# Optimization experiments

Measured on AMD Instinct MI355X. Metric: run time of the kernel, lower is better.

Reference implementation:

```python
import jax, jax.numpy as jnp
import numpy as np

N, A_IN, A_OUT, X_IN, X_OUT, NNODE = 4, 8, 16, 64, 64, 1024


def setup_inputs() -> dict:
    key = jax.random.key(0)
    ks = jax.random.split(key, 32)
    s = 0.02
    inp = {
        'A': jax.random.normal(ks[0], (N, A_IN, NNODE, NNODE), jnp.float32),
        'X': jax.random.normal(ks[1], (N, NNODE, X_IN), jnp.float32),
    }
    # Linear weights stored as (in, out); torch Linear computes x @ W.T with W (out,in)
    for i, k in zip(range(1, 6), ks[2:7]):
        inp[f'A_W{i}'] = jax.random.normal(k, (A_IN, A_OUT), jnp.float32) * s
    inp['A_W6'] = jax.random.normal(ks[7], (X_IN, A_OUT), jnp.float32) * s
    inp['A_W7'] = jax.random.normal(ks[8], (X_IN, A_OUT), jnp.float32) * s
    inp['A_bias'] = jnp.zeros((A_OUT,), jnp.float32)
    for pfx, base in (('X1', 9), ('X2', 16)):
        inp[f'{pfx}_W1'] = jax.random.normal(ks[base], (X_IN, X_OUT), jnp.float32) * s
        inp[f'{pfx}_W2'] = jax.random.normal(ks[base + 1], (X_IN, X_OUT), jnp.float32) * s
        for j in range(3, 7):
            inp[f'{pfx}_W{j}'] = jax.random.normal(ks[base + j - 1], (A_IN, X_OUT), jnp.float32) * s
        inp[f'{pfx}_bias'] = jnp.zeros((X_OUT,), jnp.float32)
    inp['out_W'] = jax.random.normal(ks[23], (A_OUT * X_OUT, X_OUT), jnp.float32) * s
    inp['out_b'] = jnp.zeros((X_OUT,), jnp.float32)
    return inp


def reference(A, X, A_W1, A_W2, A_W3, A_W4, A_W5, A_W6, A_W7, A_bias,
              X1_W1, X1_W2, X1_W3, X1_W4, X1_W5, X1_W6, X1_bias,
              X2_W1, X2_W2, X2_W3, X2_W4, X2_W5, X2_W6, X2_bias,
              out_W, out_b):
    n = A.shape[-1]
    # diag_part: N, n, 1, A_in
    dp = jnp.transpose(jnp.diagonal(A, axis1=-2, axis2=-1), (0, 2, 1))[:, :, None, :]
    mdp = jnp.mean(dp, axis=1, keepdims=True)                 # N,1,1,A_in
    moc = jnp.transpose(jnp.mean(A, axis=-1), (0, 2, 1))[:, :, None, :]  # N,n,1,A_in
    mall = jnp.mean(moc, axis=1, keepdims=True)               # N,1,1,A_in
    mX = jnp.mean(X, axis=-2, keepdims=True)                  # N,1,x_in

    At = jnp.transpose(A, (0, 2, 3, 1)) @ A_W1                # N,n,n,A_out
    At = At + mall @ A_W2
    t3 = moc @ A_W3                                           # N,n,1,A_out (linear commutes with symmetrize)
    At = At + t3 + jnp.swapaxes(t3, 1, 2)
    t6 = X @ A_W6                                             # N,n,A_out
    At = At + t6[:, :, None, :] + t6[:, None, :, :]
    At = At + (mX @ A_W7)[:, None, :, :]
    At = At + A_bias
    At = At + mdp @ A_W4
    t5 = dp @ A_W5
    At = At + t5 + jnp.swapaxes(t5, 1, 2)

    def x_branch(W1, W2, W3, W4, W5, W6, b):
        r = X @ W1 + mX @ W2 + moc[:, :, 0, :] @ W3 + mall[:, 0, :, :] @ W6 + b
        return r + dp[:, :, 0, :] @ W4 + mdp[:, 0, :, :] @ W5  # N,n,x_out

    X1t = x_branch(X1_W1, X1_W2, X1_W3, X1_W4, X1_W5, X1_W6, X1_bias)
    X2t = x_branch(X2_W1, X2_W2, X2_W3, X2_W4, X2_W5, X2_W6, X2_bias)

    out = jnp.einsum('nijs,njt->nist', At, X2t) / n           # N,n,A_out,x_out
    out = out.reshape(out.shape[0], out.shape[1], -1) @ out_W + out_b
    out = out + X1t
    return jnp.transpose(At, (0, 3, 1, 2)), out
```

## Files before the change

### kernel.cpp

```cpp
#include <hip/hip_runtime.h>


#define NB 4
#define CI 8
#define SO 16
#define XD 64
#define NN 1024

typedef unsigned short u16;
typedef unsigned int u32;
typedef float f32x4 __attribute__((ext_vector_type(4)));
typedef short bf16x8 __attribute__((ext_vector_type(8)));

#define WS_MOC    0x000000u
#define WS_DP     0x020000u
#define WS_CONSTA 0x043000u
#define WS_CX1    0x044000u
#define WS_CX2    0x045000u
#define WS_K1     0x048000u
#define WS_C2     0x04C000u
#define WS_PAIRA  0x050000u
#define WS_PAIRAT 0x090000u
#define WS_X1T    0x0D0000u
#define WS_X2TT   0x1D0000u
#define WS_WGT    0x250000u
#define WS_H      0x260000u
#define WS_XPART  0x264000u
#define WS_S2     0x268000u

__device__ __forceinline__ float bf2f(u16 u){ return __uint_as_float(((u32)u) << 16); }
__device__ __forceinline__ u16 f2bf(float f){
    u32 x = __float_as_uint(f);
    x += 0x7fffu + ((x >> 16) & 1u);
    return (u16)(x >> 16);
}

__global__ __launch_bounds__(256) void k_rowstats(const float* __restrict__ A,
                                                  const float* __restrict__ X,
                                                  float* __restrict__ moc,
                                                  float* __restrict__ dpv,
                                                  float* __restrict__ Xpart)
{
    if (blockIdx.x < NB*CI*NN/4) {
        int wave = threadIdx.x >> 6, lane = threadIdx.x & 63;
        int row = blockIdx.x * 4 + wave;
        int i = row & (NN - 1);
        const float* rp = A + (size_t)row * NN;
        f32x4 v0 = *(const f32x4*)(rp + lane * 16);
        f32x4 v1 = *(const f32x4*)(rp + lane * 16 + 4);
        f32x4 v2 = *(const f32x4*)(rp + lane * 16 + 8);
        f32x4 v3 = *(const f32x4*)(rp + lane * 16 + 12);
        float s = 0.f;
        #pragma unroll
        for (int e = 0; e < 4; e++) s += v0[e] + v1[e] + v2[e] + v3[e];
        #pragma unroll
        for (int off = 32; off; off >>= 1) s += __shfl_down(s, off);
        if (lane == 0) {
            moc[row] = s * (1.f / NN);
            dpv[row] = rp[i];
        }
    } else {
        int idx = blockIdx.x - NB*CI*NN/4;
        int b = idx >> 4, seg = idx & 15;
        int g = threadIdx.x >> 6, x = threadIdx.x & 63;
        __shared__ float red[4][64];
        float s = 0.f;
        #pragma unroll
        for (int k = 0; k < 16; k++) {
            int i = seg*64 + g*16 + k;
            s += X[((size_t)b*NN + i)*XD + x];
        }
        red[g][x] = s;
        __syncthreads();
        if (threadIdx.x < 64)
            Xpart[idx*64 + threadIdx.x] =
                red[0][threadIdx.x]+red[1][threadIdx.x]+red[2][threadIdx.x]+red[3][threadIdx.x];
    }
}

__global__ __launch_bounds__(256) void k_batchstats(
    const float* __restrict__ Xpart,
    const float* __restrict__ moc, const float* __restrict__ dpv,
    const float* __restrict__ AW2, const float* __restrict__ AW4, const float* __restrict__ AW7,
    const float* __restrict__ Abias,
    const float* __restrict__ X1W2, const float* __restrict__ X1W5, const float* __restrict__ X1W6,
    const float* __restrict__ X1b,
    const float* __restrict__ X2W2, const float* __restrict__ X2W5, const float* __restrict__ X2W6,
    const float* __restrict__ X2b,
    float* __restrict__ constA_o, float* __restrict__ cx1_o, float* __restrict__ cx2_o)
{
    int b = blockIdx.x, tid = threadIdx.x;
    __shared__ float sdp[8][32], smoc[8][32];
    __shared__ float mdp_s[8], mall_s[8], mx_s[64];
    {
        int c = tid >> 5, rr = tid & 31;
        float pd = 0.f, pm = 0.f;
        for (int i = rr; i < NN; i += 32) {
            pd += dpv[(b*CI + c)*NN + i];
            pm += moc[(b*CI + c)*NN + i];
        }
        sdp[c][rr] = pd; smoc[c][rr] = pm;
    }
    if (tid < 64) {
        float px = 0.f;
        #pragma unroll
        for (int s = 0; s < 16; s++) px += Xpart[(b*16 + s)*64 + tid];
        mx_s[tid] = px * (1.f/NN);
    }
    __syncthreads();
    if (tid < 8) {
        float sd = 0.f, sm = 0.f;
        for (int k = 0; k < 32; k++) { sd += sdp[tid][k]; sm += smoc[tid][k]; }
        mdp_s[tid] = sd * (1.f/NN); mall_s[tid] = sm * (1.f/NN);
    }
    __syncthreads();
    if (tid < SO) {
        float v = Abias[tid];
        #pragma unroll
        for (int c = 0; c < 8; c++)
            v += mall_s[c]*AW2[c*SO+tid] + mdp_s[c]*AW4[c*SO+tid];
        for (int x = 0; x < 64; x++) v += mx_s[x]*AW7[x*SO+tid];
        constA_o[b*SO + tid] = v;
    }
    if (tid < 64) {
        float v1 = X1b[tid], v2 = X2b[tid];
        for (int x = 0; x < 64; x++) {
            float m = mx_s[x];
            v1 += m*X1W2[x*64+tid];
            v2 += m*X2W2[x*64+tid];
        }
        #pragma unroll
        for (int c = 0; c < 8; c++) {
            v1 += mall_s[c]*X1W6[c*64+tid] + mdp_s[c]*X1W5[c*64+tid];
            v2 += mall_s[c]*X2W6[c*64+tid] + mdp_s[c]*X2W5[c*64+tid];
        }
        cx1_o[b*64+tid] = v1; cx2_o[b*64+tid] = v2;
    }
}

__global__ __launch_bounds__(256) void k_rows(const float* __restrict__ X,
    const float* __restrict__ moc, const float* __restrict__ dpv,
    const float* __restrict__ AW3, const float* __restrict__ AW5, const float* __restrict__ AW6,
    const float* __restrict__ X1W1, const float* __restrict__ X1W3, const float* __restrict__ X1W4,
    const float* __restrict__ X2W1, const float* __restrict__ X2W3, const float* __restrict__ X2W4,
    const float* __restrict__ cx1, const float* __restrict__ cx2,
    float* __restrict__ X1t, u16* __restrict__ X2tT,
    float* __restrict__ pairA, float* __restrict__ pairAT)
{
    int wave = threadIdx.x >> 6, u = threadIdx.x & 63;
    int r = blockIdx.x * 4 + wave;
    int b = r >> 10, i = r & (NN - 1);
    float xv = X[(size_t)r*XD + u];
    float a1 = cx1[b*XD + u], a2 = cx2[b*XD + u];
    int s = u & 15;
    float pa = 0.f;
    for (int x = 0; x < XD; x++) {
        float xx = __shfl(xv, x);
        a1 += xx * X1W1[x*XD + u];
        a2 += xx * X2W1[x*XD + u];
        pa += xx * AW6[x*SO + s];
    }
    #pragma unroll
    for (int c = 0; c < CI; c++) {
        float mv = moc[(b*CI + c)*NN + i];
        float dv = dpv[(b*CI + c)*NN + i];
        a1 += mv*X1W3[c*XD+u] + dv*X1W4[c*XD+u];
        a2 += mv*X2W3[c*XD+u] + dv*X2W4[c*XD+u];
        pa += mv*AW3[c*SO+s] + dv*AW5[c*SO+s];
    }
    X1t[(size_t)r*XD + u] = a1;
    X2tT[((size_t)b*XD + u)*NN + i] = f2bf(a2);
    if (u < SO) {
        pairA[(size_t)r*SO + u] = pa;
        pairAT[((size_t)b*SO + u)*NN + i] = pa;
    }
}

__global__ __launch_bounds__(256) void k_H(const float* __restrict__ pairAT,
                                           const u16* __restrict__ X2tT,
                                           float* __restrict__ H, float* __restrict__ s2)
{
    __shared__ float red[4][64];
    int tid = threadIdx.x;
    int t = tid & 63, g = tid >> 6;
    if (blockIdx.x < 64) {
        int b = blockIdx.x >> 4, s = blockIdx.x & 15;
        const u16* x2 = X2tT + ((size_t)(b*XD) + t)*NN;
        const float* par = pairAT + ((size_t)(b*SO) + s)*NN;
        float h = 0.f;
        for (int i = g*256; i < (g+1)*256; i += 8) {
            bf16x8 v = __builtin_bit_cast(bf16x8, *(const uint4*)(x2 + i));
            f32x4 p0 = *(const f32x4*)(par + i);
            f32x4 p1 = *(const f32x4*)(par + i + 4);
            #pragma unroll
            for (int e = 0; e < 4; e++)
                h += p0[e]*bf2f((u16)v[e]) + p1[e]*bf2f((u16)v[e+4]);
        }
        red[g][t] = h;
        __syncthreads();
        if (tid < 64)
            H[((size_t)(b*SO) + s)*64 + tid] = red[0][tid]+red[1][tid]+red[2][tid]+red[3][tid];
    } else {
        int b = blockIdx.x - 64;
        const u16* x2 = X2tT + ((size_t)(b*XD) + t)*NN;
        float p = 0.f;
        for (int i = g*256; i < (g+1)*256; i += 8) {
            bf16x8 v = __builtin_bit_cast(bf16x8, *(const uint4*)(x2 + i));
            #pragma unroll
            for (int e = 0; e < 8; e++) p += bf2f((u16)v[e]);
        }
        red[g][t] = p;
        __syncthreads();
        if (tid < 64)
            s2[b*64 + tid] = red[0][tid]+red[1][tid]+red[2][tid]+red[3][tid];
    }
}

__global__ __launch_bounds__(256) void k_small2(const float* __restrict__ Wo, const float* __restrict__ AW1,
    const float* __restrict__ constA, const float* __restrict__ H, const float* __restrict__ s2,
    float* __restrict__ K1, float* __restrict__ C2, u16* __restrict__ WGT)
{
    int tid = threadIdx.x;
    if (blockIdx.x < 4) {
        int b = blockIdx.x;
        __shared__ float ls[4][64];
        int t = tid & 63, g = tid >> 6;
        const float* s2b = s2 + b*64;
        float pc = 0.f;
        #pragma unroll
        for (int si = 0; si < 4; si++) {
            int s = g*4 + si;
            float ca = constA[b*SO + s];
            const float* Hs = H + ((size_t)(b*SO) + s)*64;
            float v = 0.f;
            for (int tt = 0; tt < 64; tt++) {
                float w = Wo[(s*64+tt)*64 + t];
                v  += s2b[tt] * w;
                pc += (Hs[tt] + ca*s2b[tt]) * w;
            }
            K1[((size_t)(b*SO) + s)*XD + t] = v;
        }
        ls[g][t] = pc;
        __syncthreads();
        if (tid < 64) C2[b*XD + tid] = (ls[0][tid]+ls[1][tid]+ls[2][tid]+ls[3][tid]) * (1.f/NN);
    } else {
        int o = (blockIdx.x - 4)*256 + tid;
        int u = o >> 9;
        int k = o & 511;
        int c = k >> 6, t = k & 63;
        float v = 0.f;
        #pragma unroll
        for (int s = 0; s < SO; s++) v += AW1[c*SO+s] * Wo[(s*64+t)*64 + u];
        WGT[(size_t)u*512 + k] = f2bf(v);
    }
}

__global__ __launch_bounds__(512, 2) void k_fused(
    const float* __restrict__ A, const u16* __restrict__ X2tT,
    const float* __restrict__ AW1,
    const float* __restrict__ pairA, const float* __restrict__ pairAT,
    const float* __restrict__ constA,
    const u16* __restrict__ WGT, const float* __restrict__ K1,
    const float* __restrict__ C2, const float* __restrict__ X1t,
    const float* __restrict__ outb,
    float* __restrict__ out0, float* __restrict__ out1)
{
    __shared__ __align__(16) char Abuf[16384];
    __shared__ __align__(16) char X2buf[8192];
    __shared__ __align__(16) float PATs[SO][64];
    __shared__ float W1s[CI][SO];

    int tid = threadIdx.x;
    int wave = tid >> 6, lane = tid & 63;
    int lr = lane & 15, lq = lane >> 4;
    int cp = wave & 3, ksh = wave >> 2;
    int iw = wave;
    int b = blockIdx.x >> 7;
    int i0 = (blockIdx.x & 127) * 8;

    if (tid < CI*SO) W1s[tid >> 4][tid & 15] = AW1[tid];

    float rc[SO];
    {
        const float* pr = pairA + ((size_t)(b*NN) + i0 + iw)*SO;
        const float* ca = constA + b*SO;
        #pragma unroll
        for (int q = 0; q < 4; q++) {
            f32x4 t4 = *(const f32x4*)(pr + q*4);
            #pragma unroll
            for (int e = 0; e < 4; e++) rc[q*4+e] = t4[e] + ca[q*4+e];
        }
    }

    f32x4 acc[4];
    #pragma unroll
    for (int nt = 0; nt < 4; nt++) acc[nt] = (f32x4){0.f,0.f,0.f,0.f};

    uint4 rA0, rA1, rX;
    uint2 rP;
    int rrA = tid >> 4;
    int rrB = 32 + rrA;
    int cbA = (tid & 15) * 16;
    int ttS = tid >> 3;
    int cbX = (tid & 7) * 16;
    int spS = tid >> 5;
    int cbP = (tid & 31) * 8;

#define STAGE_LOAD(CH) { \
    int jb_ = (CH)*64; \
    rA0 = *(const uint4*)(A + (((size_t)(b*CI + (rrA>>3)))*NN + i0 + (rrA&7))*NN + jb_ + (tid&15)*4); \
    rA1 = *(const uint4*)(A + (((size_t)(b*CI + (rrB>>3)))*NN + i0 + (rrB&7))*NN + jb_ + (tid&15)*4); \
    rX  = *(const uint4*)(X2tT + ((size_t)(b*XD) + ttS)*NN + jb_ + (tid&7)*8); \
    rP  = *(const uint2*)(pairAT + ((size_t)(b*SO) + spS)*NN + jb_ + (tid&31)*2); \
}

#define STAGE_WRITE() { \
    *(uint4*)(Abuf + rrA*256 + (cbA ^ ((rrA&7)<<4))) = rA0; \
    *(uint4*)(Abuf + rrB*256 + (cbA ^ ((rrB&7)<<4))) = rA1; \
    *(uint4*)(X2buf + ttS*128 + (cbX ^ ((ttS&7)<<4))) = rX; \
    *(uint2*)((char*)PATs + spS*256 + cbP) = rP; \
}

    STAGE_LOAD(0);

    for (int ch = 0; ch < 16; ch++) {
        __syncthreads();
        STAGE_WRITE();
        __syncthreads();
        if (ch < 15) STAGE_LOAD(ch + 1);

        int jb = ch * 64;

        {
            int rr = cp*16 + lr;
            int swz = (rr & 7) << 4;
            int y0 = ksh*128 + lq*32;
            f32x4 A0 = __builtin_bit_cast(f32x4, *(const uint4*)(Abuf + rr*256 + (y0 ^ swz)));
            f32x4 A1 = __builtin_bit_cast(f32x4, *(const uint4*)(Abuf + rr*256 + ((y0 + 16) ^ swz)));
            bf16x8 af;
            #pragma unroll
            for (int e = 0; e < 4; e++) { af[e] = (short)f2bf(A0[e]); af[e+4] = (short)f2bf(A1[e]); }
            #pragma unroll
            for (int nt = 0; nt < 4; nt++) {
                int tt = nt*16 + lr;
                bf16x8 bfr = __builtin_bit_cast(bf16x8,
                    *(const uint4*)(X2buf + tt*128 + ((ksh*64 + lq*16) ^ ((tt&7)<<4))));
                acc[nt] = __builtin_amdgcn_mfma_f32_16x16x32_bf16(af, bfr, acc[nt], 0, 0, 0);
            }
        }

        {
            float o[SO];
            #pragma unroll
            for (int s = 0; s < SO; s++) o[s] = rc[s] + PATs[s][lane];
            int swzi = iw << 4;
            #pragma unroll
            for (int c = 0; c < CI; c++) {
                float aA = *(const float*)(Abuf + (c*8 + iw)*256 + ((lane*4) ^ swzi));
                f32x4 w0 = *(const f32x4*)&W1s[c][0];
                f32x4 w1 = *(const f32x4*)&W1s[c][4];
                f32x4 w2 = *(const f32x4*)&W1s[c][8];
                f32x4 w3 = *(const f32x4*)&W1s[c][12];
                #pragma unroll
                for (int e = 0; e < 4; e++) {
                    o[e]    = fmaf(aA, w0[e], o[e]);
                    o[4+e]  = fmaf(aA, w1[e], o[4+e]);
                    o[8+e]  = fmaf(aA, w2[e], o[8+e]);
                    o[12+e] = fmaf(aA, w3[e], o[12+e]);
                }
            }
            #pragma unroll
            for (int s = 0; s < SO; s++)
                out0[((size_t)(b*SO + s)*NN + i0 + iw)*NN + jb + lane] = o[s];
        }
    }

    __syncthreads();
    if (ksh == 1) {
        #pragma unroll
        for (int nt = 0; nt < 4; nt++)
            *(f32x4*)(Abuf + (((cp*64 + lane)*16) + nt*4)*4) = acc[nt];
    }
    __syncthreads();
    f32x4 gsum[4];
    if (ksh == 0) {
        #pragma unroll
        for (int nt = 0; nt < 4; nt++) {
            f32x4 g = *(const f32x4*)(Abuf + (((cp*64 + lane)*16) + nt*4)*4);
            #pragma unroll
            for (int e = 0; e < 4; e++) g[e] += acc[nt][e];
            gsum[nt] = g;
        }
    }
    __syncthreads();

    u16* Gb = (u16*)Abuf;
    *(uint4*)(Abuf + 8192 + tid*16) = (uint4){0u,0u,0u,0u};
    if (ksh == 0) {
        #pragma unroll
        for (int nt = 0; nt < 4; nt++)
            #pragma unroll
            for (int reg = 0; reg < 4; reg++) {
                int m = lq*4 + reg;
                int c = 2*cp + (m >> 3);
                Gb[(m & 7)*512 + c*64 + nt*16 + lr] = f2bf(gsum[nt][reg]);
            }
    }
    __syncthreads();

    if (wave < 4) {
        int nt = wave;
        f32x4 acc1 = (f32x4){0.f,0.f,0.f,0.f};
        #pragma unroll
        for (int k0 = 0; k0 < 512; k0 += 32) {
            bf16x8 ga = __builtin_bit_cast(bf16x8, *(const uint4*)&Gb[lr*512 + k0 + lq*8]);
            bf16x8 wb = __builtin_bit_cast(bf16x8,
                *(const uint4*)(WGT + (size_t)(nt*16 + lr)*512 + k0 + lq*8));
            acc1 = __builtin_amdgcn_mfma_f32_16x16x32_bf16(ga, wb, acc1, 0, 0, 0);
        }
        if (lq < 2) {
            int u = nt*16 + lr;
            float k1c[SO];
            #pragma unroll
            for (int s = 0; s < SO; s++) k1c[s] = K1[((size_t)(b*SO) + s)*XD + u];
            float cb = C2[b*XD + u] + outb[u];
            #pragma unroll
            for (int reg = 0; reg < 4; reg++) {
                int ii = i0 + lq*4 + reg;
                const float* pa = pairA + ((size_t)(b*NN) + ii)*SO;
                float s16 = 0.f;
                #pragma unroll
                for (int s = 0; s < SO; s++) s16 += pa[s] * k1c[s];
                out1[((size_t)(b*NN) + ii)*XD + u] =
                    (acc1[reg] + s16) * (1.f/NN) + cb
                    + X1t[((size_t)(b*NN) + ii)*XD + u];
            }
        }
    }
#undef STAGE_LOAD
#undef STAGE_WRITE
}

extern "C" void kernel_launch(void* const* d_in, const int* in_sizes, int n_in,
                              void* d_out, int out_size, void* d_ws, size_t ws_size,
                              hipStream_t stream)
{
    const float* A     = (const float*)d_in[0];
    const float* X     = (const float*)d_in[1];
    const float* AW1   = (const float*)d_in[2];
    const float* AW2   = (const float*)d_in[3];
    const float* AW3   = (const float*)d_in[4];
    const float* AW4   = (const float*)d_in[5];
    const float* AW5   = (const float*)d_in[6];
    const float* AW6   = (const float*)d_in[7];
    const float* AW7   = (const float*)d_in[8];
    const float* Abias = (const float*)d_in[9];
    const float* X1W1  = (const float*)d_in[10];
    const float* X1W2  = (const float*)d_in[11];
    const float* X1W3  = (const float*)d_in[12];
    const float* X1W4  = (const float*)d_in[13];
    const float* X1W5  = (const float*)d_in[14];
    const float* X1W6  = (const float*)d_in[15];
    const float* X1b   = (const float*)d_in[16];
    const float* X2W1  = (const float*)d_in[17];
    const float* X2W2  = (const float*)d_in[18];
    const float* X2W3  = (const float*)d_in[19];
    const float* X2W4  = (const float*)d_in[20];
    const float* X2W5  = (const float*)d_in[21];
    const float* X2W6  = (const float*)d_in[22];
    const float* X2b   = (const float*)d_in[23];
    const float* Wo    = (const float*)d_in[24];
    const float* outb  = (const float*)d_in[25];

    char* ws = (char*)d_ws;
    float* moc    = (float*)(ws + WS_MOC);
    float* dpv    = (float*)(ws + WS_DP);
    float* constA = (float*)(ws + WS_CONSTA);
    float* cx1    = (float*)(ws + WS_CX1);
    float* cx2    = (float*)(ws + WS_CX2);
    float* K1     = (float*)(ws + WS_K1);
    float* C2     = (float*)(ws + WS_C2);
    float* pairA  = (float*)(ws + WS_PAIRA);
    float* pairAT = (float*)(ws + WS_PAIRAT);
    float* X1t    = (float*)(ws + WS_X1T);
    u16*   X2tT   = (u16*)(ws + WS_X2TT);
    u16*   WGT    = (u16*)(ws + WS_WGT);
    float* H      = (float*)(ws + WS_H);
    float* Xpart  = (float*)(ws + WS_XPART);
    float* s2     = (float*)(ws + WS_S2);

    float* out0 = (float*)d_out;
    float* out1 = out0 + (size_t)NB*SO*NN*NN;

    k_rowstats<<<dim3(NB*CI*NN/4 + 64), dim3(256), 0, stream>>>(A, X, moc, dpv, Xpart);
    k_batchstats<<<dim3(NB), dim3(256), 0, stream>>>(Xpart, moc, dpv,
        AW2, AW4, AW7, Abias, X1W2, X1W5, X1W6, X1b, X2W2, X2W5, X2W6, X2b,
        constA, cx1, cx2);
    k_rows<<<dim3(NB*NN/4), dim3(256), 0, stream>>>(X, moc, dpv,
        AW3, AW5, AW6, X1W1, X1W3, X1W4, X2W1, X2W3, X2W4, cx1, cx2,
        X1t, X2tT, pairA, pairAT);
    k_H<<<dim3(68), dim3(256), 0, stream>>>(pairAT, X2tT, H, s2);
    k_small2<<<dim3(132), dim3(256), 0, stream>>>(Wo, AW1, constA, H, s2, K1, C2, WGT);
    k_fused<<<dim3(NB*NN/8), dim3(512), 0, stream>>>(A, X2tT, AW1,
        pairA, pairAT, constA, WGT, K1, C2, X1t, outb, out0, out1);
}
```

Baseline: 510.6 us.

## Double-buffer LDS stages in fused kernel and move WGT build into k_H

The fused main kernel now keeps two LDS buffers for the A, X2 and pairAT chunks. The next chunk is written into the alternate buffer after compute, which removes one of the two barriers per iteration. Separately, the WGT weight-product computation moves from k_small2 into extra blocks of k_H, so it runs alongside the H reductions and k_small2 shrinks to 4 blocks. Doubling shared memory (about 25KB to 50KB per block) may limit how many 512-thread blocks fit per CU.

Result: no change. 502.4 us (-1.6%).

```diff
diff --git a/kernel.cpp b/kernel.cpp
--- a/kernel.cpp
+++ b/kernel.cpp
@@ -178,7 +178,9 @@
 
 __global__ __launch_bounds__(256) void k_H(const float* __restrict__ pairAT,
                                            const u16* __restrict__ X2tT,
-                                           float* __restrict__ H, float* __restrict__ s2)
+                                           const float* __restrict__ Wo, const float* __restrict__ AW1,
+                                           float* __restrict__ H, float* __restrict__ s2,
+                                           u16* __restrict__ WGT)
 {
     __shared__ float red[4][64];
     int tid = threadIdx.x;
@@ -200,7 +202,7 @@
         __syncthreads();
         if (tid < 64)
             H[((size_t)(b*SO) + s)*64 + tid] = red[0][tid]+red[1][tid]+red[2][tid]+red[3][tid];
-    } else {
+    } else if (blockIdx.x < 68) {
         int b = blockIdx.x - 64;
         const u16* x2 = X2tT + ((size_t)(b*XD) + t)*NN;
         float p = 0.f;
@@ -213,46 +215,44 @@
         __syncthreads();
         if (tid < 64)
             s2[b*64 + tid] = red[0][tid]+red[1][tid]+red[2][tid]+red[3][tid];
-    }
-}
-
-__global__ __launch_bounds__(256) void k_small2(const float* __restrict__ Wo, const float* __restrict__ AW1,
-    const float* __restrict__ constA, const float* __restrict__ H, const float* __restrict__ s2,
-    float* __restrict__ K1, float* __restrict__ C2, u16* __restrict__ WGT)
-{
-    int tid = threadIdx.x;
-    if (blockIdx.x < 4) {
-        int b = blockIdx.x;
-        __shared__ float ls[4][64];
-        int t = tid & 63, g = tid >> 6;
-        const float* s2b = s2 + b*64;
-        float pc = 0.f;
-        #pragma unroll
-        for (int si = 0; si < 4; si++) {
-            int s = g*4 + si;
-            float ca = constA[b*SO + s];
-            const float* Hs = H + ((size_t)(b*SO) + s)*64;
-            float v = 0.f;
-            for (int tt = 0; tt < 64; tt++) {
-                float w = Wo[(s*64+tt)*64 + t];
-                v  += s2b[tt] * w;
-                pc += (Hs[tt] + ca*s2b[tt]) * w;
-            }
-            K1[((size_t)(b*SO) + s)*XD + t] = v;
-        }
-        ls[g][t] = pc;
-        __syncthreads();
-        if (tid < 64) C2[b*XD + tid] = (ls[0][tid]+ls[1][tid]+ls[2][tid]+ls[3][tid]) * (1.f/NN);
     } else {
-        int o = (blockIdx.x - 4)*256 + tid;
+        int o = (blockIdx.x - 68)*256 + tid;
         int u = o >> 9;
         int k = o & 511;
-        int c = k >> 6, t = k & 63;
+        int c = k >> 6, tt = k & 63;
         float v = 0.f;
         #pragma unroll
-        for (int s = 0; s < SO; s++) v += AW1[c*SO+s] * Wo[(s*64+t)*64 + u];
+        for (int s = 0; s < SO; s++) v += AW1[c*SO+s] * Wo[(s*64+tt)*64 + u];
         WGT[(size_t)u*512 + k] = f2bf(v);
     }
+}
+
+__global__ __launch_bounds__(256) void k_small2(const float* __restrict__ Wo,
+    const float* __restrict__ constA, const float* __restrict__ H, const float* __restrict__ s2,
+    float* __restrict__ K1, float* __restrict__ C2)
+{
+    int tid = threadIdx.x;
+    int b = blockIdx.x;
+    __shared__ float ls[4][64];
+    int t = tid & 63, g = tid >> 6;
+    const float* s2b = s2 + b*64;
+    float pc = 0.f;
+    #pragma unroll
+    for (int si = 0; si < 4; si++) {
+        int s = g*4 + si;
+        float ca = constA[b*SO + s];
+        const float* Hs = H + ((size_t)(b*SO) + s)*64;
+        float v = 0.f;
+        for (int tt = 0; tt < 64; tt++) {
+            float w = Wo[(s*64+tt)*64 + t];
+            v  += s2b[tt] * w;
+            pc += (Hs[tt] + ca*s2b[tt]) * w;
+        }
+        K1[((size_t)(b*SO) + s)*XD + t] = v;
+    }
+    ls[g][t] = pc;
+    __syncthreads();
+    if (tid < 64) C2[b*XD + tid] = (ls[0][tid]+ls[1][tid]+ls[2][tid]+ls[3][tid]) * (1.f/NN);
 }
 
 __global__ __launch_bounds__(512, 2) void k_fused(
@@ -265,9 +265,9 @@
     const float* __restrict__ outb,
     float* __restrict__ out0, float* __restrict__ out1)
 {
-    __shared__ __align__(16) char Abuf[16384];
-    __shared__ __align__(16) char X2buf[8192];
-    __shared__ __align__(16) float PATs[SO][64];
+    __shared__ __align__(16) char AbufD[2][16384];
+    __shared__ __align__(16) char X2bufD[2][8192];
+    __shared__ __align__(16) float PATsD[2][SO][64];
     __shared__ float W1s[CI][SO];
 
     int tid = threadIdx.x;
@@ -314,21 +314,23 @@
     rP  = *(const uint2*)(pairAT + ((size_t)(b*SO) + spS)*NN + jb_ + (tid&31)*2); \
 }
 
-#define STAGE_WRITE() { \
-    *(uint4*)(Abuf + rrA*256 + (cbA ^ ((rrA&7)<<4))) = rA0; \
-    *(uint4*)(Abuf + rrB*256 + (cbA ^ ((rrB&7)<<4))) = rA1; \
-    *(uint4*)(X2buf + ttS*128 + (cbX ^ ((ttS&7)<<4))) = rX; \
-    *(uint2*)((char*)PATs + spS*256 + cbP) = rP; \
+#define STAGE_WRITE(BUF) { \
+    char* Ab_ = AbufD[BUF]; \
+    *(uint4*)(Ab_ + rrA*256 + (cbA ^ ((rrA&7)<<4))) = rA0; \
+    *(uint4*)(Ab_ + rrB*256 + (cbA ^ ((rrB&7)<<4))) = rA1; \
+    *(uint4*)(X2bufD[BUF] + ttS*128 + (cbX ^ ((ttS&7)<<4))) = rX; \
+    *(uint2*)((char*)PATsD[BUF] + spS*256 + cbP) = rP; \
 }
 
     STAGE_LOAD(0);
+    STAGE_WRITE(0);
+    __syncthreads();
 
     for (int ch = 0; ch < 16; ch++) {
-        __syncthreads();
-        STAGE_WRITE();
-        __syncthreads();
+        int cur = ch & 1;
         if (ch < 15) STAGE_LOAD(ch + 1);
-
+        const char* Abuf = AbufD[cur];
+        const char* X2buf = X2bufD[cur];
         int jb = ch * 64;
 
         {
@@ -352,7 +354,7 @@
         {
             float o[SO];
             #pragma unroll
-            for (int s = 0; s < SO; s++) o[s] = rc[s] + PATs[s][lane];
+            for (int s = 0; s < SO; s++) o[s] = rc[s] + PATsD[cur][s][lane];
             int swzi = iw << 4;
             #pragma unroll
             for (int c = 0; c < CI; c++) {
@@ -373,20 +375,23 @@
             for (int s = 0; s < SO; s++)
                 out0[((size_t)(b*SO + s)*NN + i0 + iw)*NN + jb + lane] = o[s];
         }
-    }
-
-    __syncthreads();
+
+        if (ch < 15) STAGE_WRITE(cur ^ 1);
+        __syncthreads();
+    }
+
+    char* Gbase = AbufD[0];
     if (ksh == 1) {
         #pragma unroll
         for (int nt = 0; nt < 4; nt++)
-            *(f32x4*)(Abuf + (((cp*64 + lane)*16) + nt*4)*4) = acc[nt];
+            *(f32x4*)(Gbase + (((cp*64 + lane)*16) + nt*4)*4) = acc[nt];
     }
     __syncthreads();
     f32x4 gsum[4];
     if (ksh == 0) {
         #pragma unroll
         for (int nt = 0; nt < 4; nt++) {
-            f32x4 g = *(const f32x4*)(Abuf + (((cp*64 + lane)*16) + nt*4)*4);
+            f32x4 g = *(const f32x4*)(Gbase + (((cp*64 + lane)*16) + nt*4)*4);
             #pragma unroll
             for (int e = 0; e < 4; e++) g[e] += acc[nt][e];
             gsum[nt] = g;
@@ -394,8 +399,8 @@
     }
     __syncthreads();
 
-    u16* Gb = (u16*)Abuf;
-    *(uint4*)(Abuf + 8192 + tid*16) = (uint4){0u,0u,0u,0u};
+    u16* Gb = (u16*)Gbase;
+    *(uint4*)(Gbase + 8192 + tid*16) = (uint4){0u,0u,0u,0u};
     if (ksh == 0) {
         #pragma unroll
         for (int nt = 0; nt < 4; nt++)
@@ -499,8 +504,8 @@
     k_rows<<<dim3(NB*NN/4), dim3(256), 0, stream>>>(X, moc, dpv,
         AW3, AW5, AW6, X1W1, X1W3, X1W4, X2W1, X2W3, X2W4, cx1, cx2,
         X1t, X2tT, pairA, pairAT);
-    k_H<<<dim3(68), dim3(256), 0, stream>>>(pairAT, X2tT, H, s2);
-    k_small2<<<dim3(132), dim3(256), 0, stream>>>(Wo, AW1, constA, H, s2, K1, C2, WGT);
+    k_H<<<dim3(196), dim3(256), 0, stream>>>(pairAT, X2tT, Wo, AW1, H, s2, WGT);
+    k_small2<<<dim3(4), dim3(256), 0, stream>>>(Wo, constA, H, s2, K1, C2);
     k_fused<<<dim3(NB*NN/8), dim3(512), 0, stream>>>(A, X2tT, AW1,
         pairA, pairAT, constA, WGT, K1, C2, X1t, outb, out0, out1);
 }
```
